# Kernel optimization log

Measured on AMD Instinct MI355X. Metric: run time of the kernel, lower is better.

The kernel has to match this reference:

```python
import jax, jax.numpy as jnp
import numpy as np

B, H, L, D = 256, 1024, 10000, 8  # batch, hidden, num_labels, expert hidden

def setup_inputs() -> dict:
    key = jax.random.key(0)
    k1, k2, k3, k4, k5 = jax.random.split(key, 5)
    scale1 = 1.0 / np.sqrt(H)
    scale2 = 1.0 / np.sqrt(D)
    return {
        "embeddings": jax.random.normal(k1, (B, H), dtype=jnp.float32),
        "W1": jax.random.normal(k2, (L, H, D), dtype=jnp.float32) * scale1,
        "b1": jax.random.normal(k3, (L, D), dtype=jnp.float32) * scale1,
        "W2": jax.random.normal(k4, (L, D), dtype=jnp.float32) * scale2,
        "b2": jax.random.normal(k5, (L,), dtype=jnp.float32) * scale2,
    }

def reference(embeddings, W1, b1, W2, b2):
    # Fused batched-GEMM form of the Python loop over L tiny MLPs:
    # per-label Linear(H->8) -> ReLU -> Linear(8->1), concatenated along labels.
    h = jnp.einsum('bh,lhd->bld', embeddings, W1) + b1[None, :, :]  # [B, L, 8]
    h = jax.nn.relu(h)
    logits = jnp.einsum('bld,ld->bl', h, W2) + b2[None, :]          # [B, L]
    return logits
```

## Files before the change

kernel.cpp:

```cpp
#include <hip/hip_runtime.h>
#include <stdint.h>
#include <stddef.h>


#define B_ 256
#define H_ 1024
#define L_ 10000
#define D_ 8
#define NL 8
#define KB 32
#define NSTEP (H_ / KB)

typedef __bf16 bf16_t;
typedef bf16_t bf16x8 __attribute__((ext_vector_type(8)));
typedef float f32x4 __attribute__((ext_vector_type(4)));
typedef int i32x4 __attribute__((ext_vector_type(4)));

__device__ __forceinline__ uint32_t cvt_pk_bf16(float lo, float hi) {
  uint32_t a = __builtin_bit_cast(uint32_t, lo);
  uint32_t b = __builtin_bit_cast(uint32_t, hi);
  a += 0x7FFFu + ((a >> 16) & 1u);
  b += 0x7FFFu + ((b >> 16) & 1u);
  return (a >> 16) | (b & 0xFFFF0000u);
}

__device__ __forceinline__ void gl_lds16(const void* g, void* l) {
  __builtin_amdgcn_global_load_lds(
      (const __attribute__((address_space(1))) uint32_t*)g,
      (__attribute__((address_space(3))) uint32_t*)l, 16, 0, 0);
}

__global__ void imec_prep(const float* __restrict__ E, uint8_t* __restrict__ Ebf) {
  const int t = blockIdx.x * blockDim.x + threadIdx.x;
  const int m = t >> 7;
  const int cg = t & 127;
  const int kb = cg >> 2;
  const int c = cg & 3;
  const float* src = E + (size_t)m * H_ + kb * KB + c * 8;
  f32x4 x = *(const f32x4*)src;
  f32x4 y = *(const f32x4*)(src + 4);
  i32x4 v;
  v[0] = cvt_pk_bf16(x[0], x[1]);
  v[1] = cvt_pk_bf16(x[2], x[3]);
  v[2] = cvt_pk_bf16(y[0], y[1]);
  v[3] = cvt_pk_bf16(y[2], y[3]);
  const int cp = c ^ ((m >> 1) & 3);
  *(i32x4*)(Ebf + ((size_t)kb << 14) + (m << 6) + (cp << 4)) = v;
}

template <bool USE_WS>
__global__ __launch_bounds__(256, 2) void imec_main(
    const float* __restrict__ E, const float* __restrict__ W1,
    const float* __restrict__ b1, const float* __restrict__ W2,
    const float* __restrict__ b2, float* __restrict__ out,
    const uint8_t* __restrict__ Ebf) {
  __shared__ alignas(16) uint8_t sE[16384];
  __shared__ alignas(16) uint8_t sW[4096];

  const int tid = threadIdx.x;
  const int w = tid >> 6;
  const int lane = tid & 63;
  const int wg = blockIdx.x;
  const int n = lane & 15;
  const int q = lane >> 4;

  const int d_st = n & 7;
  const int lp_st = n >> 3;
  const long label_st = (long)wg * NL + w * 2 + lp_st;
  const float* w1p = W1 + label_st * (long)(H_ * D_) + (q * 8) * D_ + d_st;

  f32x4 acc[4][4];
#pragma unroll
  for (int i = 0; i < 4; ++i)
#pragma unroll
    for (int j = 0; j < 4; ++j) acc[i][j] = (f32x4){0.f, 0.f, 0.f, 0.f};

  float r[8];
#pragma unroll
  for (int j = 0; j < 8; ++j) r[j] = w1p[j * D_];
  w1p += KB * D_;

  const int sw = (n >> 1) & 3;

  for (int kb = 0; kb < NSTEP; ++kb) {
    if constexpr (USE_WS) {
      asm volatile("s_barrier" ::: "memory");
    } else {
      __syncthreads();
    }

    if constexpr (USE_WS) {
#pragma unroll
      for (int i = 0; i < 4; ++i) {
        const uint8_t* g =
            Ebf + ((size_t)kb << 14) + (w << 12) + (i << 10) + (lane << 4);
        gl_lds16(g, sE + (w << 12) + (i << 10));
      }
    } else {
      const int m = tid;
      const f32x4* er = (const f32x4*)(E + (size_t)m * H_ + kb * KB);
#pragma unroll
      for (int c = 0; c < 4; ++c) {
        f32x4 x = er[2 * c];
        f32x4 y = er[2 * c + 1];
        i32x4 v;
        v[0] = cvt_pk_bf16(x[0], x[1]);
        v[1] = cvt_pk_bf16(x[2], x[3]);
        v[2] = cvt_pk_bf16(y[0], y[1]);
        v[3] = cvt_pk_bf16(y[2], y[3]);
        *(i32x4*)(sE + (m << 6) + ((c ^ ((m >> 1) & 3)) << 4)) = v;
      }
    }

    {
      i32x4 v;
      v[0] = cvt_pk_bf16(r[0], r[1]);
      v[1] = cvt_pk_bf16(r[2], r[3]);
      v[2] = cvt_pk_bf16(r[4], r[5]);
      v[3] = cvt_pk_bf16(r[6], r[7]);
      *(i32x4*)(sW + (w << 10) + (lane << 4)) = v;
    }

    if constexpr (USE_WS) {
      __builtin_amdgcn_sched_barrier(0);
      if (kb + 1 < NSTEP) {
#pragma unroll
        for (int j = 0; j < 8; ++j) r[j] = w1p[j * D_];
        w1p += KB * D_;
        __builtin_amdgcn_sched_barrier(0);
        asm volatile("s_waitcnt vmcnt(8) lgkmcnt(0)\n\t"
                     "s_barrier" ::: "memory");
      } else {
        asm volatile("s_waitcnt vmcnt(0) lgkmcnt(0)\n\t"
                     "s_barrier" ::: "memory");
      }
    } else {
      __syncthreads();
      if (kb + 1 < NSTEP) {
#pragma unroll
        for (int j = 0; j < 8; ++j) r[j] = w1p[j * D_];
        w1p += KB * D_;
      }
    }

    bf16x8 bfr[4];
#pragma unroll
    for (int t = 0; t < 4; ++t)
      bfr[t] = *(const bf16x8*)(sW + (t << 10) + (lane << 4));
    bf16x8 afr[4];
#pragma unroll
    for (int mt = 0; mt < 4; ++mt) {
      const int ml = w * 64 + mt * 16 + n;
      afr[mt] = *(const bf16x8*)(sE + (ml << 6) + ((q ^ sw) << 4));
    }

#pragma unroll
    for (int mt = 0; mt < 4; ++mt)
#pragma unroll
      for (int t = 0; t < 4; ++t)
        acc[mt][t] = __builtin_amdgcn_mfma_f32_16x16x32_bf16(
            afr[mt], bfr[t], acc[mt][t], 0, 0, 0);
  }

#pragma unroll
  for (int t = 0; t < 4; ++t) {
    const int label = wg * NL + t * 2 + lp_st;
    const float b1v = b1[label * D_ + d_st];
    const float w2v = W2[label * D_ + d_st];
    const float b2v = b2[label];
#pragma unroll
    for (int mt = 0; mt < 4; ++mt) {
#pragma unroll
      for (int rr = 0; rr < 4; ++rr) {
        float v = acc[mt][t][rr] + b1v;
        v = fmaxf(v, 0.f) * w2v;
        v += __shfl_xor(v, 1);
        v += __shfl_xor(v, 2);
        v += __shfl_xor(v, 4);
        if ((lane & 7) == 0) {
          const int m = w * 64 + mt * 16 + q * 4 + rr;
          out[(size_t)m * L_ + label] = v + b2v;
        }
      }
    }
  }
}

extern "C" void kernel_launch(void* const* d_in, const int* in_sizes, int n_in,
                              void* d_out, int out_size, void* d_ws,
                              size_t ws_size, hipStream_t stream) {
  const float* E = (const float*)d_in[0];
  const float* W1 = (const float*)d_in[1];
  const float* b1 = (const float*)d_in[2];
  const float* W2 = (const float*)d_in[3];
  const float* b2 = (const float*)d_in[4];
  float* out = (float*)d_out;

  const size_t need = (size_t)B_ * H_ * 2;
  if (ws_size >= need) {
    uint8_t* Ebf = (uint8_t*)d_ws;
    imec_prep<<<(B_ * H_ / 8) / 256, 256, 0, stream>>>(E, Ebf);
    imec_main<true><<<L_ / NL, 256, 0, stream>>>(E, W1, b1, W2, b2, out, Ebf);
  } else {
    imec_main<false><<<L_ / NL, 256, 0, stream>>>(E, W1, b1, W2, b2, out,
                                                  nullptr);
  }
}
```

Baseline: 493.0 us.

## Double-buffer embedding tiles in LDS and vectorize W1 loads with scattered bf16 stores

Embedding tiles now go into two LDS buffers, so the next k-step's global-to-LDS copy is issued before the current step's MFMAs and overlaps them rather than waiting behind a barrier. W1 is read with coalesced 16-byte vector loads per lane, two labels per wave, instead of eight strided scalar loads. The values are then converted and scattered into sW as individual 16-bit stores to rebuild the MFMA B-fragment layout. This doubles LDS use for sE (which may affect occupancy at two blocks per CU) and adds many small LDS writes. The vmcnt wait count is adjusted to match the new number of outstanding loads.

```diff
diff --git a/kernel.cpp b/kernel.cpp
--- a/kernel.cpp
+++ b/kernel.cpp
@@ -22,6 +22,12 @@
   a += 0x7FFFu + ((a >> 16) & 1u);
   b += 0x7FFFu + ((b >> 16) & 1u);
   return (a >> 16) | (b & 0xFFFF0000u);
+}
+
+__device__ __forceinline__ uint16_t cvt1_bf16(float x) {
+  uint32_t a = __builtin_bit_cast(uint32_t, x);
+  a += 0x7FFFu + ((a >> 16) & 1u);
+  return (uint16_t)(a >> 16);
 }
 
 __device__ __forceinline__ void gl_lds16(const void* g, void* l) {
@@ -54,7 +60,7 @@
     const float* __restrict__ b1, const float* __restrict__ W2,
     const float* __restrict__ b2, float* __restrict__ out,
     const uint8_t* __restrict__ Ebf) {
-  __shared__ alignas(16) uint8_t sE[16384];
+  __shared__ alignas(16) uint8_t sE[32768];
   __shared__ alignas(16) uint8_t sW[4096];
 
   const int tid = threadIdx.x;
@@ -64,10 +70,14 @@
   const int n = lane & 15;
   const int q = lane >> 4;
 
-  const int d_st = n & 7;
-  const int lp_st = n >> 3;
-  const long label_st = (long)wg * NL + w * 2 + lp_st;
-  const float* w1p = W1 + label_st * (long)(H_ * D_) + (q * 8) * D_ + d_st;
+  const int lab0 = wg * NL + w * 2;
+  const float* p0 = W1 + (size_t)lab0 * (H_ * D_) + lane * 4;
+  const float* p1 = p0 + (H_ * D_);
+
+  const int rrow = lane >> 1;
+  const int dq = lane & 1;
+  const int wbase = (w << 9) + ((rrow >> 3) << 7) + (dq << 5) + (rrow & 7);
+  uint16_t* sW16 = (uint16_t*)sW;
 
   f32x4 acc[4][4];
 #pragma unroll
@@ -75,28 +85,41 @@
 #pragma unroll
     for (int j = 0; j < 4; ++j) acc[i][j] = (f32x4){0.f, 0.f, 0.f, 0.f};
 
-  float r[8];
-#pragma unroll
-  for (int j = 0; j < 8; ++j) r[j] = w1p[j * D_];
-  w1p += KB * D_;
-
   const int sw = (n >> 1) & 3;
 
+  f32x4 r0, r1, rn0, rn1;
+
+  if constexpr (USE_WS) {
+#pragma unroll
+    for (int i = 0; i < 4; ++i) {
+      const uint8_t* g = Ebf + (w << 12) + (i << 10) + (lane << 4);
+      gl_lds16(g, sE + (w << 12) + (i << 10));
+    }
+    __builtin_amdgcn_sched_barrier(0);
+  }
+  r0 = *(const f32x4*)p0;
+  r1 = *(const f32x4*)p1;
+  if constexpr (USE_WS) __builtin_amdgcn_sched_barrier(0);
+
   for (int kb = 0; kb < NSTEP; ++kb) {
+    const int eb = kb & 1;
+
     if constexpr (USE_WS) {
       asm volatile("s_barrier" ::: "memory");
+      if (kb + 1 < NSTEP) {
+#pragma unroll
+        for (int i = 0; i < 4; ++i) {
+          const uint8_t* g = Ebf + (((size_t)(kb + 1)) << 14) + (w << 12) +
+                             (i << 10) + (lane << 4);
+          gl_lds16(g, sE + ((1 - eb) << 14) + (w << 12) + (i << 10));
+        }
+        __builtin_amdgcn_sched_barrier(0);
+        rn0 = *(const f32x4*)(p0 + (size_t)(kb + 1) * (KB * D_));
+        rn1 = *(const f32x4*)(p1 + (size_t)(kb + 1) * (KB * D_));
+        __builtin_amdgcn_sched_barrier(0);
+      }
     } else {
       __syncthreads();
-    }
-
-    if constexpr (USE_WS) {
-#pragma unroll
-      for (int i = 0; i < 4; ++i) {
-        const uint8_t* g =
-            Ebf + ((size_t)kb << 14) + (w << 12) + (i << 10) + (lane << 4);
-        gl_lds16(g, sE + (w << 12) + (i << 10));
-      }
-    } else {
       const int m = tid;
       const f32x4* er = (const f32x4*)(E + (size_t)m * H_ + kb * KB);
 #pragma unroll
@@ -110,39 +133,29 @@
         v[3] = cvt_pk_bf16(y[2], y[3]);
         *(i32x4*)(sE + (m << 6) + ((c ^ ((m >> 1) & 3)) << 4)) = v;
       }
-    }
-
-    {
-      i32x4 v;
-      v[0] = cvt_pk_bf16(r[0], r[1]);
-      v[1] = cvt_pk_bf16(r[2], r[3]);
-      v[2] = cvt_pk_bf16(r[4], r[5]);
-      v[3] = cvt_pk_bf16(r[6], r[7]);
-      *(i32x4*)(sW + (w << 10) + (lane << 4)) = v;
-    }
+      if (kb + 1 < NSTEP) {
+        rn0 = *(const f32x4*)(p0 + (size_t)(kb + 1) * (KB * D_));
+        rn1 = *(const f32x4*)(p1 + (size_t)(kb + 1) * (KB * D_));
+      }
+    }
+
+#pragma unroll
+    for (int i = 0; i < 4; ++i) sW16[wbase + i * 8] = cvt1_bf16(r0[i]);
+#pragma unroll
+    for (int i = 0; i < 4; ++i) sW16[wbase + 64 + i * 8] = cvt1_bf16(r1[i]);
 
     if constexpr (USE_WS) {
-      __builtin_amdgcn_sched_barrier(0);
-      if (kb + 1 < NSTEP) {
-#pragma unroll
-        for (int j = 0; j < 8; ++j) r[j] = w1p[j * D_];
-        w1p += KB * D_;
-        __builtin_amdgcn_sched_barrier(0);
-        asm volatile("s_waitcnt vmcnt(8) lgkmcnt(0)\n\t"
+      if (kb + 1 < NSTEP)
+        asm volatile("s_waitcnt vmcnt(6) lgkmcnt(0)\n\t"
                      "s_barrier" ::: "memory");
-      } else {
+      else
         asm volatile("s_waitcnt vmcnt(0) lgkmcnt(0)\n\t"
                      "s_barrier" ::: "memory");
-      }
     } else {
       __syncthreads();
-      if (kb + 1 < NSTEP) {
-#pragma unroll
-        for (int j = 0; j < 8; ++j) r[j] = w1p[j * D_];
-        w1p += KB * D_;
-      }
-    }
-
+    }
+
+    const uint8_t* sEb = sE + (USE_WS ? (eb << 14) : 0);
     bf16x8 bfr[4];
 #pragma unroll
     for (int t = 0; t < 4; ++t)
@@ -151,7 +164,7 @@
 #pragma unroll
     for (int mt = 0; mt < 4; ++mt) {
       const int ml = w * 64 + mt * 16 + n;
-      afr[mt] = *(const bf16x8*)(sE + (ml << 6) + ((q ^ sw) << 4));
+      afr[mt] = *(const bf16x8*)(sEb + (ml << 6) + ((q ^ sw) << 4));
     }
 
 #pragma unroll
@@ -160,8 +173,15 @@
       for (int t = 0; t < 4; ++t)
         acc[mt][t] = __builtin_amdgcn_mfma_f32_16x16x32_bf16(
             afr[mt], bfr[t], acc[mt][t], 0, 0, 0);
-  }
-
+
+    if (kb + 1 < NSTEP) {
+      r0 = rn0;
+      r1 = rn1;
+    }
+  }
+
+  const int d_st = n & 7;
+  const int lp_st = n >> 3;
 #pragma unroll
   for (int t = 0; t < 4; ++t) {
     const int label = wg * NL + t * 2 + lp_st;
```

Measured after the change: 490.1 us. About the same (-0.6%).
